# Optimization experiments

Measured on AMD Instinct MI355X. Metric: run time of the kernel, lower is better.

## Reference

```python
import jax, jax.numpy as jnp
import numpy as np


def setup_inputs() -> dict:
    key = jax.random.key(0)
    ks = jax.random.split(key, 6)
    S, B, E = 2048, 2, 1024
    scale = 1.0 / np.sqrt(E)
    return {
        "query": jax.random.normal(ks[0], (S, B, E), dtype=jnp.float32),
        "key": jax.random.normal(ks[1], (S, B, E), dtype=jnp.float32),
        "value": jax.random.normal(ks[2], (S, B, E), dtype=jnp.float32),
        "in_proj_w": jax.random.normal(ks[3], (3 * E, E), dtype=jnp.float32) * scale,
        "in_proj_b": jnp.zeros((3 * E,), dtype=jnp.float32),
        "out_proj_w": jax.random.normal(ks[4], (E, E), dtype=jnp.float32) * scale,
        "out_proj_b": jnp.zeros((E,), dtype=jnp.float32),
        "num_heads": 16,
        "block_size": 128,
    }


def reference(query, key, value, in_proj_w, in_proj_b, out_proj_w, out_proj_b,
              num_heads, block_size):
    # Shapes: query/key/value [S, B, E] (torch MHA default, batch_first=False)
    S, B, E = query.shape
    H = num_heads
    D = E // H

    wq, wk, wv = jnp.split(in_proj_w, 3, axis=0)   # each [E, E]
    bq, bk, bv = jnp.split(in_proj_b, 3, axis=0)   # each [E]

    def proj(x, w, b):
        # [S,B,E] @ [E,E]^T + b -> [B,H,S,D]
        y = x @ w.T + b
        return y.reshape(S, B, H, D).transpose(1, 2, 0, 3)

    q = proj(query, wq, bq) * (1.0 / np.sqrt(D))
    k = proj(key, wk, bk)
    v = proj(value, wv, bv)

    # Dense scores with banded mask: allowed iff i-block <= j <= i+block-1
    scores = jnp.einsum("bhsd,bhtd->bhst", q, k)  # [B,H,S,S]
    i = jnp.arange(S)[:, None]
    j = jnp.arange(S)[None, :]
    allowed = (j >= i - block_size) & (j < i + block_size)  # [S,S]
    neg_inf = jnp.asarray(-jnp.inf, dtype=scores.dtype)
    scores = jnp.where(allowed[None, None], scores, neg_inf)

    attn = jax.nn.softmax(scores, axis=-1)
    ctx = jnp.einsum("bhst,bhtd->bhsd", attn, v)           # [B,H,S,D]
    ctx = ctx.transpose(2, 0, 1, 3).reshape(S, B, E)       # [S,B,E]
    return ctx @ out_proj_w.T + out_proj_b
```

## Files before the change

kernel.cpp:

```cpp
#include <hip/hip_runtime.h>
#include <hip/hip_bf16.h>

#define S_LEN 2048
#define BATCH 2
#define EMB   1024
#define NHEAD 16
#define HDIM  64
#define WIN   128

typedef __attribute__((ext_vector_type(8))) short short8;
typedef __attribute__((ext_vector_type(4))) float floatx4;

__device__ __forceinline__ unsigned int pk2bf(float a, float b) {
    unsigned int ua = __builtin_bit_cast(unsigned int, a);
    unsigned int ub = __builtin_bit_cast(unsigned int, b);
    ua += 0x7fffu + ((ua >> 16) & 1u);
    ub += 0x7fffu + ((ub >> 16) & 1u);
    return (ua >> 16) | (ub & 0xffff0000u);
}
__device__ __forceinline__ unsigned short f2bf(float f) {
    unsigned int u = __builtin_bit_cast(unsigned int, f);
    u += 0x7fffu + ((u >> 16) & 1u);
    return (unsigned short)(u >> 16);
}

__device__ __forceinline__ void gl_lds16(const unsigned short* g, unsigned short* l) {
    __builtin_amdgcn_global_load_lds(
        (const __attribute__((address_space(1))) unsigned int*)g,
        (__attribute__((address_space(3))) unsigned int*)l,
        16, 0, 0);
}

#define QKV_UNITS 524288
#define WI_UNITS  393216
#define WO_UNITS  131072

__global__ __launch_bounds__(256)
void convert_kernel(const float* __restrict__ xq, const float* __restrict__ xk,
                    const float* __restrict__ xv, const float* __restrict__ wi,
                    const float* __restrict__ wo,
                    unsigned short* __restrict__ xqb, unsigned short* __restrict__ xkb,
                    unsigned short* __restrict__ xvb, unsigned short* __restrict__ wib,
                    unsigned short* __restrict__ wob)
{
    const size_t u = (size_t)blockIdx.x * 256 + threadIdx.x;
    const float* src;
    unsigned short* dst;
    size_t off;
    if (u < 3 * (size_t)QKV_UNITS) {
        const int which = (int)(u / QKV_UNITS);
        off = (u % QKV_UNITS) * 8;
        src = (which == 0) ? xq : (which == 1) ? xk : xv;
        dst = (which == 0) ? xqb : (which == 1) ? xkb : xvb;
    } else if (u < 3 * (size_t)QKV_UNITS + WI_UNITS) {
        off = (u - 3 * (size_t)QKV_UNITS) * 8;
        src = wi; dst = wib;
    } else {
        off = (u - (3 * (size_t)QKV_UNITS + WI_UNITS)) * 8;
        src = wo; dst = wob;
    }
    float4 a = *reinterpret_cast<const float4*>(src + off);
    float4 b = *reinterpret_cast<const float4*>(src + off + 4);
    uint4 p = {pk2bf(a.x, a.y), pk2bf(a.z, a.w), pk2bf(b.x, b.y), pk2bf(b.z, b.w)};
    *reinterpret_cast<uint4*>(dst + off) = p;
}

__global__ __launch_bounds__(256)
void qkv_gemm_kernel(const unsigned short* __restrict__ xqb,
                     const unsigned short* __restrict__ xkb,
                     const unsigned short* __restrict__ xvb,
                     const unsigned short* __restrict__ wib,
                     const float* __restrict__ bias,
                     unsigned short* __restrict__ qo,
                     unsigned short* __restrict__ ko,
                     unsigned short* __restrict__ vto)
{
    __shared__ unsigned short SM[8192];
    unsigned short* As = SM;
    unsigned short* Bs = SM + 4096;

    const int bid  = blockIdx.x;
    const int which = bid >> 8;
    const int bx   = (bid >> 5) & 7;
    const int by   = bid & 31;

    const unsigned short* A = (which == 0) ? xqb : (which == 1) ? xkb : xvb;
    const unsigned short* W = wib + (size_t)which * EMB * EMB;
    const float* bv = bias + which * EMB;
    const float scale = (which == 0) ? 0.125f : 1.0f;

    const int tid  = threadIdx.x;
    const int lane = tid & 63;
    const int wave = tid >> 6;
    const int quad = lane >> 4;
    const int c16  = lane & 15;
    const int wm   = (wave & 1) << 6;
    const int wn   = (wave >> 1) << 6;

    const int rowBase = by * 128;
    const int colBase = bx * 128;

    const int lrow = lane >> 2;
    const int lseg = (((lane & 3) ^ (lrow & 3)) << 3);

    floatx4 acc[4][4];
    #pragma unroll
    for (int i = 0; i < 4; ++i)
        #pragma unroll
        for (int j = 0; j < 4; ++j)
            acc[i][j] = (floatx4){0.f, 0.f, 0.f, 0.f};

    const int rxor = c16 & 3;
    const int soff = ((quad ^ rxor) << 3);

    for (int k0 = 0; k0 < EMB; k0 += 32) {
        __syncthreads();
        #pragma unroll
        for (int t = 0; t < 2; ++t) {
            const int c = wave * 2 + t;
            const int row = c * 16 + lrow;
            gl_lds16(A + (size_t)(rowBase + row) * EMB + k0 + lseg, &As[c * 512]);
            gl_lds16(W + (size_t)(colBase + row) * EMB + k0 + lseg, &Bs[c * 512]);
        }
        __syncthreads();

        short8 af[4], bf[4];
        #pragma unroll
        for (int mi = 0; mi < 4; ++mi)
            af[mi] = *reinterpret_cast<const short8*>(
                &As[(wm + mi * 16 + c16) * 32 + soff]);
        #pragma unroll
        for (int ni = 0; ni < 4; ++ni)
            bf[ni] = *reinterpret_cast<const short8*>(
                &Bs[(wn + ni * 16 + c16) * 32 + soff]);

        #pragma unroll
        for (int mi = 0; mi < 4; ++mi)
            #pragma unroll
            for (int ni = 0; ni < 4; ++ni)
                acc[mi][ni] = __builtin_amdgcn_mfma_f32_16x16x32_bf16(
                    af[mi], bf[ni], acc[mi][ni], 0, 0, 0);
    }

    if (which != 2) {
        #pragma unroll
        for (int ni = 0; ni < 4; ++ni) {
            const int n_full = colBase + wn + ni * 16 + c16;
            const float bb = bv[n_full];
            const int h = n_full >> 6;
            const int d = n_full & 63;
            #pragma unroll
            for (int mi = 0; mi < 4; ++mi) {
                #pragma unroll
                for (int r = 0; r < 4; ++r) {
                    const int m_g = rowBase + wm + mi * 16 + quad * 4 + r;
                    const int s   = m_g >> 1;
                    const int b   = m_g & 1;
                    const int bh  = b * NHEAD + h;
                    const unsigned short val = f2bf((acc[mi][ni][r] + bb) * scale);
                    if (which == 0)
                        qo[((size_t)bh * S_LEN + s) * HDIM + d] = val;
                    else
                        ko[((size_t)bh * S_LEN + s) * HDIM + d] = val;
                }
            }
        }
    } else {
        for (int p = 0; p < 2; ++p) {
            __syncthreads();
            if ((wn >> 6) == p) {
                #pragma unroll
                for (int ni = 0; ni < 4; ++ni) {
                    const int n_loc2 = ni * 16 + c16;
                    const int n_full = colBase + p * 64 + n_loc2;
                    const float bb = bv[n_full];
                    const int k2 = (n_loc2 & 3) << 4;
                    #pragma unroll
                    for (int mi = 0; mi < 4; ++mi) {
                        #pragma unroll
                        for (int r = 0; r < 4; ++r) {
                            const int m_local = wm + mi * 16 + quad * 4 + r;
                            const int lin = (m_local & 1) * 64 + (m_local >> 1);
                            SM[n_loc2 * 128 + (lin ^ k2)] = f2bf(acc[mi][ni][r] + bb);
                        }
                    }
                }
            }
            __syncthreads();
            const int nlp = tid & 63;
            const int b   = (tid >> 6) & 1;
            const int sh  = tid >> 7;
            const int k2  = (nlp & 3) << 4;
            const int n_full = colBase + p * 64 + nlp;
            const int h = n_full >> 6;
            const int d = n_full & 63;
            const int bh = b * NHEAD + h;
            unsigned short* dst = vto + ((size_t)bh * HDIM + d) * S_LEN
                                      + (rowBase >> 1) + sh * 32;
            #pragma unroll
            for (int g = 0; g < 4; ++g) {
                const uint4 vv = *reinterpret_cast<const uint4*>(
                    &SM[nlp * 128 + ((b * 64 + sh * 32 + g * 8) ^ k2)]);
                *reinterpret_cast<uint4*>(dst + g * 8) = vv;
            }
        }
    }
}

#define AT_STRIDE 72

__global__ __launch_bounds__(256)
void attn_mfma_kernel(const unsigned short* __restrict__ q,
                      const unsigned short* __restrict__ k,
                      const unsigned short* __restrict__ vt,
                      unsigned short* __restrict__ ctx)
{
    __shared__ unsigned short Qs[64 * AT_STRIDE];
    __shared__ unsigned short Ks[64 * AT_STRIDE];
    __shared__ unsigned short Vts[64 * AT_STRIDE];
    __shared__ unsigned short Ps[64 * AT_STRIDE];

    const int bid = blockIdx.x;
    const int bh  = bid & 31;
    const int s0  = (bid >> 5) * 64;
    const int tid = threadIdx.x;
    const int lane = tid & 63;
    const int wave = tid >> 6;
    const int quad = lane >> 4;
    const int c16  = lane & 15;

    const size_t base_qk = ((size_t)bh * S_LEN) * HDIM;
    const size_t base_vt = ((size_t)bh * HDIM) * S_LEN;

    const int srow = tid >> 2;
    const int sseg = (tid & 3) << 4;
    {
        const unsigned short* src = q + base_qk + (size_t)(s0 + srow) * HDIM + sseg;
        uint4 v0 = *reinterpret_cast<const uint4*>(src);
        uint4 v1 = *reinterpret_cast<const uint4*>(src + 8);
        *reinterpret_cast<uint4*>(&Qs[srow * AT_STRIDE + sseg])     = v0;
        *reinterpret_cast<uint4*>(&Qs[srow * AT_STRIDE + sseg + 8]) = v1;
    }

    float m_ = -1.0e30f, l_ = 0.f;
    floatx4 ob[4];
    #pragma unroll
    for (int dt = 0; dt < 4; ++dt) ob[dt] = (floatx4){0.f, 0.f, 0.f, 0.f};

    const int qg = s0 + wave * 16 + c16;

    int c0 = s0 - 128; if (c0 < 0) c0 = 0;
    int c1 = s0 + 192; if (c1 > S_LEN) c1 = S_LEN;

    uint4 k0v, k1v, v0v, v1v;
#define LOADKV(CB)                                                                \
    {                                                                             \
        const unsigned short* ksrc = k + base_qk + (size_t)((CB) + srow) * HDIM + sseg; \
        const unsigned short* vsrc = vt + base_vt + (size_t)srow * S_LEN + (CB) + sseg; \
        k0v = *reinterpret_cast<const uint4*>(ksrc);                              \
        k1v = *reinterpret_cast<const uint4*>(ksrc + 8);                          \
        v0v = *reinterpret_cast<const uint4*>(vsrc);                              \
        v1v = *reinterpret_cast<const uint4*>(vsrc + 8);                          \
    }

    LOADKV(c0);

    for (int cb = c0; cb < c1; cb += 64) {
        __syncthreads();
        *reinterpret_cast<uint4*>(&Ks[srow * AT_STRIDE + sseg])      = k0v;
        *reinterpret_cast<uint4*>(&Ks[srow * AT_STRIDE + sseg + 8])  = k1v;
        *reinterpret_cast<uint4*>(&Vts[srow * AT_STRIDE + sseg])     = v0v;
        *reinterpret_cast<uint4*>(&Vts[srow * AT_STRIDE + sseg + 8]) = v1v;
        __syncthreads();
        if (cb + 64 < c1) LOADKV(cb + 64);

        floatx4 sc[4];
        #pragma unroll
        for (int jt = 0; jt < 4; ++jt) sc[jt] = (floatx4){0.f, 0.f, 0.f, 0.f};
        {
            short8 af0 = *reinterpret_cast<const short8*>(
                &Qs[(wave * 16 + c16) * AT_STRIDE + quad * 8]);
            short8 af1 = *reinterpret_cast<const short8*>(
                &Qs[(wave * 16 + c16) * AT_STRIDE + 32 + quad * 8]);
            #pragma unroll
            for (int jt = 0; jt < 4; ++jt) {
                short8 bf0 = *reinterpret_cast<const short8*>(
                    &Ks[(jt * 16 + c16) * AT_STRIDE + quad * 8]);
                short8 bf1 = *reinterpret_cast<const short8*>(
                    &Ks[(jt * 16 + c16) * AT_STRIDE + 32 + quad * 8]);
                sc[jt] = __builtin_amdgcn_mfma_f32_16x16x32_bf16(bf0, af0, sc[jt], 0, 0, 0);
                sc[jt] = __builtin_amdgcn_mfma_f32_16x16x32_bf16(bf1, af1, sc[jt], 0, 0, 0);
            }
        }

        float rm = -3.0e38f;
        #pragma unroll
        for (int jt = 0; jt < 4; ++jt) {
            #pragma unroll
            for (int r = 0; r < 4; ++r) {
                const int jg = cb + jt * 16 + quad * 4 + r;
                float x = sc[jt][r];
                if (jg < qg - WIN || jg >= qg + WIN) x = -3.0e38f;
                sc[jt][r] = x;
                rm = fmaxf(rm, x);
            }
        }
        rm = fmaxf(rm, __shfl_xor(rm, 16));
        rm = fmaxf(rm, __shfl_xor(rm, 32));
        const float mn    = fmaxf(m_, rm);
        const float alpha = __expf(m_ - mn);
        float rs = 0.f;
        #pragma unroll
        for (int jt = 0; jt < 4; ++jt) {
            #pragma unroll
            for (int r = 0; r < 4; ++r) {
                const float p = __expf(sc[jt][r] - mn);
                sc[jt][r] = p;
                rs += p;
            }
        }
        rs += __shfl_xor(rs, 16);
        rs += __shfl_xor(rs, 32);
        l_ = l_ * alpha + rs;
        m_ = mn;

        #pragma unroll
        for (int r = 0; r < 4; ++r) {
            const float ar = __shfl(alpha, (lane & 48) | (quad * 4 + r));
            #pragma unroll
            for (int dt = 0; dt < 4; ++dt) ob[dt][r] *= ar;
        }

        #pragma unroll
        for (int jt = 0; jt < 4; ++jt) {
            uint2 pw;
            pw.x = pk2bf(sc[jt][0], sc[jt][1]);
            pw.y = pk2bf(sc[jt][2], sc[jt][3]);
            *reinterpret_cast<uint2*>(
                &Ps[(wave * 16 + c16) * AT_STRIDE + jt * 16 + quad * 4]) = pw;
        }

        {
            short8 pa0 = *reinterpret_cast<const short8*>(
                &Ps[(wave * 16 + c16) * AT_STRIDE + quad * 8]);
            short8 pa1 = *reinterpret_cast<const short8*>(
                &Ps[(wave * 16 + c16) * AT_STRIDE + 32 + quad * 8]);
            #pragma unroll
            for (int dt = 0; dt < 4; ++dt) {
                short8 bv0 = *reinterpret_cast<const short8*>(
                    &Vts[(dt * 16 + c16) * AT_STRIDE + quad * 8]);
                short8 bv1 = *reinterpret_cast<const short8*>(
                    &Vts[(dt * 16 + c16) * AT_STRIDE + 32 + quad * 8]);
                ob[dt] = __builtin_amdgcn_mfma_f32_16x16x32_bf16(pa0, bv0, ob[dt], 0, 0, 0);
                ob[dt] = __builtin_amdgcn_mfma_f32_16x16x32_bf16(pa1, bv1, ob[dt], 0, 0, 0);
            }
        }
    }
#undef LOADKV

    const int b = bh >> 4;
    const int h = bh & 15;
    #pragma unroll
    for (int r = 0; r < 4; ++r) {
        const int sg  = s0 + wave * 16 + quad * 4 + r;
        const float lr = __shfl(l_, (lane & 48) | (quad * 4 + r));
        const float inv = 1.0f / lr;
        #pragma unroll
        for (int dt = 0; dt < 4; ++dt) {
            const int d = dt * 16 + c16;
            ctx[((size_t)(sg * BATCH + b) << 10) + (h << 6) + d] = f2bf(ob[dt][r] * inv);
        }
    }
}

__global__ __launch_bounds__(256)
void out_gemm_kernel(const unsigned short* __restrict__ ctxb,
                     const unsigned short* __restrict__ wob,
                     const float* __restrict__ bias,
                     float* __restrict__ out)
{
    __shared__ unsigned short As[128 * 64];
    __shared__ unsigned short Bs[128 * 64];

    const int bid = blockIdx.x;
    const int bx  = bid >> 5;
    const int by  = bid & 31;

    const int tid  = threadIdx.x;
    const int lane = tid & 63;
    const int wave = tid >> 6;
    const int quad = lane >> 4;
    const int c16  = lane & 15;
    const int wm   = (wave & 1) << 6;
    const int wn   = (wave >> 1) << 6;

    const int rowBase = by * 128;
    const int colBase = bx * 128;

    const int lrow = lane >> 3;
    const int lseg = (((lane & 7) ^ lrow) << 3);

    floatx4 acc[4][4];
    #pragma unroll
    for (int i = 0; i < 4; ++i)
        #pragma unroll
        for (int j = 0; j < 4; ++j)
            acc[i][j] = (floatx4){0.f, 0.f, 0.f, 0.f};

    const int rxor = c16 & 7;

    for (int k0 = 0; k0 < EMB; k0 += 64) {
        __syncthreads();
        #pragma unroll
        for (int t = 0; t < 4; ++t) {
            const int c = wave * 4 + t;
            const int row = c * 8 + lrow;
            gl_lds16(ctxb + (size_t)(rowBase + row) * EMB + k0 + lseg, &As[c * 512]);
            gl_lds16(wob  + (size_t)(colBase + row) * EMB + k0 + lseg, &Bs[c * 512]);
        }
        __syncthreads();

        #pragma unroll
        for (int kk = 0; kk < 2; ++kk) {
            const int soff = (((quad + 4 * kk) ^ rxor) << 3);
            short8 af[4], bf[4];
            #pragma unroll
            for (int mi = 0; mi < 4; ++mi)
                af[mi] = *reinterpret_cast<const short8*>(
                    &As[(wm + mi * 16 + c16) * 64 + soff]);
            #pragma unroll
            for (int ni = 0; ni < 4; ++ni)
                bf[ni] = *reinterpret_cast<const short8*>(
                    &Bs[(wn + ni * 16 + c16) * 64 + soff]);

            #pragma unroll
            for (int mi = 0; mi < 4; ++mi)
                #pragma unroll
                for (int ni = 0; ni < 4; ++ni)
                    acc[mi][ni] = __builtin_amdgcn_mfma_f32_16x16x32_bf16(
                        af[mi], bf[ni], acc[mi][ni], 0, 0, 0);
        }
    }

    #pragma unroll
    for (int ni = 0; ni < 4; ++ni) {
        const int n_full = colBase + wn + ni * 16 + c16;
        const float bb = bias[n_full];
        #pragma unroll
        for (int mi = 0; mi < 4; ++mi) {
            #pragma unroll
            for (int r = 0; r < 4; ++r) {
                const int m_g = rowBase + wm + mi * 16 + quad * 4 + r;
                out[(size_t)m_g * EMB + n_full] = acc[mi][ni][r] + bb;
            }
        }
    }
}

extern "C" void kernel_launch(void* const* d_in, const int* in_sizes, int n_in,
                              void* d_out, int out_size, void* d_ws, size_t ws_size,
                              hipStream_t stream) {
    const float* query = (const float*)d_in[0];
    const float* key   = (const float*)d_in[1];
    const float* value = (const float*)d_in[2];
    const float* in_w  = (const float*)d_in[3];
    const float* in_b  = (const float*)d_in[4];
    const float* out_w = (const float*)d_in[5];
    const float* out_b = (const float*)d_in[6];

    const size_t PLANE = (size_t)BATCH * NHEAD * S_LEN * HDIM;
    unsigned short* xqb = (unsigned short*)d_ws;
    unsigned short* xkb = xqb + PLANE;
    unsigned short* xvb = xkb + PLANE;
    unsigned short* wib = xvb + PLANE;
    unsigned short* wob = wib + (size_t)3 * EMB * EMB;
    unsigned short* qo  = wob + (size_t)EMB * EMB;
    unsigned short* ko  = qo + PLANE;
    unsigned short* vto = ko + PLANE;
    unsigned short* cw  = vto + PLANE;

    convert_kernel<<<8192, 256, 0, stream>>>(query, key, value, in_w, out_w,
                                             xqb, xkb, xvb, wib, wob);

    qkv_gemm_kernel<<<768, 256, 0, stream>>>(xqb, xkb, xvb, wib, in_b, qo, ko, vto);

    attn_mfma_kernel<<<1024, 256, 0, stream>>>(qo, ko, vto, cw);

    out_gemm_kernel<<<256, 256, 0, stream>>>(cw, wob, out_b, (float*)d_out);
}
```

Before: 202.3 us.

## Simplify V-transpose epilogue, add MFMA priority hints, halve out-GEMM tile width

The QKV GEMM's LDS-staged coalesced transpose for V is replaced by direct scattered bf16 stores into the transposed V layout. s_setprio is raised around the attention MFMA loops. The output GEMM tile is cut from 128x128 to 128x64, giving 512 blocks to fill more CUs. The direct V stores write 2-byte values with a stride of S_LEN, which likely hurts write coalescing in exchange for dropping two barriers and the LDS staging.

```diff
diff --git a/kernel.cpp b/kernel.cpp
--- a/kernel.cpp
+++ b/kernel.cpp
@@ -75,9 +75,8 @@
                      unsigned short* __restrict__ ko,
                      unsigned short* __restrict__ vto)
 {
-    __shared__ unsigned short SM[8192];
-    unsigned short* As = SM;
-    unsigned short* Bs = SM + 4096;
+    __shared__ unsigned short As[128 * 32];
+    __shared__ unsigned short Bs[128 * 32];
 
     const int bid  = blockIdx.x;
     const int which = bid >> 8;
@@ -111,7 +110,6 @@
             acc[i][j] = (floatx4){0.f, 0.f, 0.f, 0.f};
 
     const int rxor = c16 & 3;
-    const int soff = ((quad ^ rxor) << 3);
 
     for (int k0 = 0; k0 < EMB; k0 += 32) {
         __syncthreads();
@@ -124,6 +122,7 @@
         }
         __syncthreads();
 
+        const int soff = ((quad ^ rxor) << 3);
         short8 af[4], bf[4];
         #pragma unroll
         for (int mi = 0; mi < 4; ++mi)
@@ -142,66 +141,27 @@
                     af[mi], bf[ni], acc[mi][ni], 0, 0, 0);
     }
 
-    if (which != 2) {
-        #pragma unroll
-        for (int ni = 0; ni < 4; ++ni) {
-            const int n_full = colBase + wn + ni * 16 + c16;
-            const float bb = bv[n_full];
-            const int h = n_full >> 6;
-            const int d = n_full & 63;
-            #pragma unroll
-            for (int mi = 0; mi < 4; ++mi) {
-                #pragma unroll
-                for (int r = 0; r < 4; ++r) {
-                    const int m_g = rowBase + wm + mi * 16 + quad * 4 + r;
-                    const int s   = m_g >> 1;
-                    const int b   = m_g & 1;
-                    const int bh  = b * NHEAD + h;
-                    const unsigned short val = f2bf((acc[mi][ni][r] + bb) * scale);
-                    if (which == 0)
-                        qo[((size_t)bh * S_LEN + s) * HDIM + d] = val;
-                    else
-                        ko[((size_t)bh * S_LEN + s) * HDIM + d] = val;
-                }
-            }
-        }
-    } else {
-        for (int p = 0; p < 2; ++p) {
-            __syncthreads();
-            if ((wn >> 6) == p) {
-                #pragma unroll
-                for (int ni = 0; ni < 4; ++ni) {
-                    const int n_loc2 = ni * 16 + c16;
-                    const int n_full = colBase + p * 64 + n_loc2;
-                    const float bb = bv[n_full];
-                    const int k2 = (n_loc2 & 3) << 4;
-                    #pragma unroll
-                    for (int mi = 0; mi < 4; ++mi) {
-                        #pragma unroll
-                        for (int r = 0; r < 4; ++r) {
-                            const int m_local = wm + mi * 16 + quad * 4 + r;
-                            const int lin = (m_local & 1) * 64 + (m_local >> 1);
-                            SM[n_loc2 * 128 + (lin ^ k2)] = f2bf(acc[mi][ni][r] + bb);
-                        }
-                    }
-                }
-            }
-            __syncthreads();
-            const int nlp = tid & 63;
-            const int b   = (tid >> 6) & 1;
-            const int sh  = tid >> 7;
-            const int k2  = (nlp & 3) << 4;
-            const int n_full = colBase + p * 64 + nlp;
-            const int h = n_full >> 6;
-            const int d = n_full & 63;
-            const int bh = b * NHEAD + h;
-            unsigned short* dst = vto + ((size_t)bh * HDIM + d) * S_LEN
-                                      + (rowBase >> 1) + sh * 32;
-            #pragma unroll
-            for (int g = 0; g < 4; ++g) {
-                const uint4 vv = *reinterpret_cast<const uint4*>(
-                    &SM[nlp * 128 + ((b * 64 + sh * 32 + g * 8) ^ k2)]);
-                *reinterpret_cast<uint4*>(dst + g * 8) = vv;
+    #pragma unroll
+    for (int ni = 0; ni < 4; ++ni) {
+        const int n_full = colBase + wn + ni * 16 + c16;
+        const float bb = bv[n_full];
+        const int h = n_full >> 6;
+        const int d = n_full & 63;
+        #pragma unroll
+        for (int mi = 0; mi < 4; ++mi) {
+            #pragma unroll
+            for (int r = 0; r < 4; ++r) {
+                const int m_g = rowBase + wm + mi * 16 + quad * 4 + r;
+                const int s   = m_g >> 1;
+                const int b   = m_g & 1;
+                const int bh  = b * NHEAD + h;
+                const unsigned short val = f2bf((acc[mi][ni][r] + bb) * scale);
+                if (which == 2)
+                    vto[((size_t)bh * HDIM + d) * S_LEN + s] = val;
+                else if (which == 0)
+                    qo[((size_t)bh * S_LEN + s) * HDIM + d] = val;
+                else
+                    ko[((size_t)bh * S_LEN + s) * HDIM + d] = val;
             }
         }
     }
@@ -282,6 +242,7 @@
                 &Qs[(wave * 16 + c16) * AT_STRIDE + quad * 8]);
             short8 af1 = *reinterpret_cast<const short8*>(
                 &Qs[(wave * 16 + c16) * AT_STRIDE + 32 + quad * 8]);
+            __builtin_amdgcn_s_setprio(1);
             #pragma unroll
             for (int jt = 0; jt < 4; ++jt) {
                 short8 bf0 = *reinterpret_cast<const short8*>(
@@ -291,6 +252,7 @@
                 sc[jt] = __builtin_amdgcn_mfma_f32_16x16x32_bf16(bf0, af0, sc[jt], 0, 0, 0);
                 sc[jt] = __builtin_amdgcn_mfma_f32_16x16x32_bf16(bf1, af1, sc[jt], 0, 0, 0);
             }
+            __builtin_amdgcn_s_setprio(0);
         }
 
         float rm = -3.0e38f;
@@ -345,6 +307,7 @@
                 &Ps[(wave * 16 + c16) * AT_STRIDE + quad * 8]);
             short8 pa1 = *reinterpret_cast<const short8*>(
                 &Ps[(wave * 16 + c16) * AT_STRIDE + 32 + quad * 8]);
+            __builtin_amdgcn_s_setprio(1);
             #pragma unroll
             for (int dt = 0; dt < 4; ++dt) {
                 short8 bv0 = *reinterpret_cast<const short8*>(
@@ -354,6 +317,7 @@
                 ob[dt] = __builtin_amdgcn_mfma_f32_16x16x32_bf16(pa0, bv0, ob[dt], 0, 0, 0);
                 ob[dt] = __builtin_amdgcn_mfma_f32_16x16x32_bf16(pa1, bv1, ob[dt], 0, 0, 0);
             }
+            __builtin_amdgcn_s_setprio(0);
         }
     }
 #undef LOADKV
@@ -380,7 +344,7 @@
                      float* __restrict__ out)
 {
     __shared__ unsigned short As[128 * 64];
-    __shared__ unsigned short Bs[128 * 64];
+    __shared__ unsigned short Bs[64 * 64];
 
     const int bid = blockIdx.x;
     const int bx  = bid >> 5;
@@ -391,18 +355,17 @@
     const int wave = tid >> 6;
     const int quad = lane >> 4;
     const int c16  = lane & 15;
-    const int wm   = (wave & 1) << 6;
-    const int wn   = (wave >> 1) << 6;
+    const int wm   = wave * 32;
 
     const int rowBase = by * 128;
-    const int colBase = bx * 128;
+    const int colBase = bx * 64;
 
     const int lrow = lane >> 3;
     const int lseg = (((lane & 7) ^ lrow) << 3);
 
-    floatx4 acc[4][4];
-    #pragma unroll
-    for (int i = 0; i < 4; ++i)
+    floatx4 acc[2][4];
+    #pragma unroll
+    for (int i = 0; i < 2; ++i)
         #pragma unroll
         for (int j = 0; j < 4; ++j)
             acc[i][j] = (floatx4){0.f, 0.f, 0.f, 0.f};
@@ -416,25 +379,30 @@
             const int c = wave * 4 + t;
             const int row = c * 8 + lrow;
             gl_lds16(ctxb + (size_t)(rowBase + row) * EMB + k0 + lseg, &As[c * 512]);
-            gl_lds16(wob  + (size_t)(colBase + row) * EMB + k0 + lseg, &Bs[c * 512]);
+        }
+        #pragma unroll
+        for (int t = 0; t < 2; ++t) {
+            const int c = wave * 2 + t;
+            const int row = c * 8 + lrow;
+            gl_lds16(wob + (size_t)(colBase + row) * EMB + k0 + lseg, &Bs[c * 512]);
         }
         __syncthreads();
 
         #pragma unroll
         for (int kk = 0; kk < 2; ++kk) {
             const int soff = (((quad + 4 * kk) ^ rxor) << 3);
-            short8 af[4], bf[4];
-            #pragma unroll
-            for (int mi = 0; mi < 4; ++mi)
+            short8 af[2], bf[4];
+            #pragma unroll
+            for (int mi = 0; mi < 2; ++mi)
                 af[mi] = *reinterpret_cast<const short8*>(
                     &As[(wm + mi * 16 + c16) * 64 + soff]);
             #pragma unroll
             for (int ni = 0; ni < 4; ++ni)
                 bf[ni] = *reinterpret_cast<const short8*>(
-                    &Bs[(wn + ni * 16 + c16) * 64 + soff]);
-
-            #pragma unroll
-            for (int mi = 0; mi < 4; ++mi)
+                    &Bs[(ni * 16 + c16) * 64 + soff]);
+
+            #pragma unroll
+            for (int mi = 0; mi < 2; ++mi)
                 #pragma unroll
                 for (int ni = 0; ni < 4; ++ni)
                     acc[mi][ni] = __builtin_amdgcn_mfma_f32_16x16x32_bf16(
@@ -444,10 +412,10 @@
 
     #pragma unroll
     for (int ni = 0; ni < 4; ++ni) {
-        const int n_full = colBase + wn + ni * 16 + c16;
+        const int n_full = colBase + ni * 16 + c16;
         const float bb = bias[n_full];
         #pragma unroll
-        for (int mi = 0; mi < 4; ++mi) {
+        for (int mi = 0; mi < 2; ++mi) {
             #pragma unroll
             for (int r = 0; r < 4; ++r) {
                 const int m_g = rowBase + wm + mi * 16 + quad * 4 + r;
@@ -486,5 +454,5 @@
 
     attn_mfma_kernel<<<1024, 256, 0, stream>>>(qo, ko, vto, cw);
 
-    out_gemm_kernel<<<256, 256, 0, stream>>>(cw, wob, out_b, (float*)d_out);
-}
+    out_gemm_kernel<<<512, 256, 0, stream>>>(cw, wob, out_b, (float*)d_out);
+}
```

Result: faster. 188.1 us (median of 2 runs) (-7.0%).
